# Optimization experiments

Hardware: AMD Instinct MI355X
Metric: run time of the kernel (lower is better)

## Reference

```python
import jax, jax.numpy as jnp
import numpy as np

N_NODES = 50000
N_PAIRS = 625000
F = 128

def setup_inputs() -> dict:
    key = jax.random.key(0)
    k1, k2, k3, k4, k5 = jax.random.split(key, 5)
    x = jax.random.normal(k1, (N_NODES, F), dtype=jnp.float32)
    alpha_ij = jax.random.normal(k2, (N_PAIRS,), dtype=jnp.float32)
    idx_i = jax.random.randint(k3, (N_PAIRS,), 0, N_NODES, dtype=jnp.int32)
    idx_j = jax.random.randint(k4, (N_PAIRS,), 0, N_NODES, dtype=jnp.int32)
    # Dense(F, use_bias=False) kernel, shape (F_in, F_out)
    W = jax.random.normal(k5, (F, F), dtype=jnp.float32) / np.sqrt(F)
    return {"x": x, "alpha_ij": alpha_ij, "idx_i": idx_i, "idx_j": idx_j, "W": W}

def reference(x, alpha_ij, idx_i, idx_j, W):
    # dense projection on nodes (n,F) @ (F,F) -> (n,F)
    v = jnp.matmul(x, W)
    # gather neighbor values, scale by attention coeff: (n_pairs, F)
    msg = alpha_ij[:, None] * v[idx_j]
    # scatter-sum back to center atoms
    return jax.ops.segment_sum(msg, segment_ids=idx_i, num_segments=x.shape[0])
```

## Files before the change

### kernel.cpp

```cpp
#include <hip/hip_runtime.h>
#include <stdint.h>

#define FDIM 128
#define BR 64
#define NB_C 782
#define QC 1152
#define PPB 2048

typedef short  s8v   __attribute__((ext_vector_type(8)));
typedef float  f4v   __attribute__((ext_vector_type(4)));
typedef unsigned short u8v __attribute__((ext_vector_type(8)));

__device__ __forceinline__ unsigned short f2bf(float f) {
    union { float f; uint32_t u; } c; c.f = f;
    uint32_t u = c.u;
    return (unsigned short)((u + 0x7fffu + ((u >> 16) & 1u)) >> 16);
}
__device__ __forceinline__ float bflo2f(uint32_t g) {
    union { uint32_t u; float f; } c; c.u = g << 16; return c.f;
}
__device__ __forceinline__ float bfhi2f(uint32_t g) {
    union { uint32_t u; float f; } c; c.u = g & 0xffff0000u; return c.f;
}

__global__ __launch_bounds__(256) void prep(const float* __restrict__ W,
                                            unsigned short* __restrict__ Wt,
                                            int* __restrict__ gcur) {
    int i = blockIdx.x * 256 + threadIdx.x;
    if (i < FDIM * FDIM) {
        int n = i & 127, k = i >> 7;
        Wt[n * FDIM + k] = f2bf(W[k * FDIM + n]);
    }
    if (i < NB_C) gcur[i] = 0;
}

__global__ __launch_bounds__(256) void fused_gemm_pass1(
        const float* __restrict__ x,
        const unsigned short* __restrict__ Wt,
        unsigned short* __restrict__ v,
        const int* __restrict__ idx_i,
        const int* __restrict__ idx_j,
        const float* __restrict__ alpha,
        int* __restrict__ gcur,
        unsigned long long* __restrict__ qrec,
        int n_rows, int n_pairs, int PB) {
    __shared__ unsigned short As[BR][FDIM + 8];

    if ((int)blockIdx.x < PB) {
        __shared__ int hist[NB_C];
        __shared__ int base_s[NB_C];
        const int t = threadIdx.x;
        const int start = blockIdx.x * PPB;

        for (int b = t; b < NB_C; b += 256) hist[b] = 0;
        __syncthreads();

        unsigned long long rec[8];
        int bkt[8];
#pragma unroll
        for (int i = 0; i < 8; ++i) {
            int p = start + t + i * 256;
            bkt[i] = -1;
            if (p < n_pairs) {
                int ii = idx_i[p];
                int b  = ii >> 6;
                bkt[i] = b;
                rec[i] = (unsigned long long)(uint32_t)(idx_j[p] | ((ii & 63) << 16))
                       | ((unsigned long long)(uint32_t)__float_as_int(alpha[p]) << 32);
                atomicAdd(&hist[b], 1);
            }
        }
        __syncthreads();
        for (int b = t; b < NB_C; b += 256) {
            int h = hist[b];
            base_s[b] = (h > 0) ? atomicAdd(&gcur[b], h) : 0;
            hist[b] = 0;
        }
        __syncthreads();
#pragma unroll
        for (int i = 0; i < 8; ++i) {
            int b = bkt[i];
            if (b >= 0) {
                int lp  = atomicAdd(&hist[b], 1);
                int pos = base_s[b] + lp;
                if (pos < QC)
                    qrec[(size_t)b * QC + pos] = rec[i];
            }
        }
        return;
    }

    const int t = threadIdx.x;
    const int row0 = (blockIdx.x - PB) * BR;
    {
        int r  = t >> 2;
        int c0 = (t & 3) * 32;
        int grow = row0 + r;
        const float* src = x + (size_t)grow * FDIM + c0;
#pragma unroll
        for (int it = 0; it < 4; ++it) {
            float4 xa = make_float4(0.f, 0.f, 0.f, 0.f);
            float4 xb = make_float4(0.f, 0.f, 0.f, 0.f);
            if (grow < n_rows) {
                xa = *(const float4*)(src + it * 8);
                xb = *(const float4*)(src + it * 8 + 4);
            }
            u8v pk;
            pk[0] = f2bf(xa.x); pk[1] = f2bf(xa.y); pk[2] = f2bf(xa.z); pk[3] = f2bf(xa.w);
            pk[4] = f2bf(xb.x); pk[5] = f2bf(xb.y); pk[6] = f2bf(xb.z); pk[7] = f2bf(xb.w);
            *(u8v*)(&As[r][c0 + it * 8]) = pk;
        }
    }
    __syncthreads();

    const int w    = t >> 6;
    const int lane = t & 63;
    const int rt   = (w & 1) * 32;
    const int ct   = (w >> 1) * 64;
    const int lrow = lane & 15;
    const int kq   = (lane >> 4) * 8;

    f4v acc[2][4];
#pragma unroll
    for (int i = 0; i < 2; ++i)
#pragma unroll
        for (int j = 0; j < 4; ++j)
            acc[i][j] = (f4v){0.f, 0.f, 0.f, 0.f};

#pragma unroll
    for (int ks = 0; ks < 4; ++ks) {
        const int k0 = ks * 32 + kq;
        const unsigned short* wb = Wt + (size_t)(ct + lrow) * FDIM + k0;
        s8v b0 = *(const s8v*)(wb);
        s8v b1 = *(const s8v*)(wb + 16 * FDIM);
        s8v b2 = *(const s8v*)(wb + 32 * FDIM);
        s8v b3 = *(const s8v*)(wb + 48 * FDIM);
        s8v a0 = *(const s8v*)(&As[rt + lrow][k0]);
        s8v a1 = *(const s8v*)(&As[rt + 16 + lrow][k0]);
        acc[0][0] = __builtin_amdgcn_mfma_f32_16x16x32_bf16(a0, b0, acc[0][0], 0, 0, 0);
        acc[0][1] = __builtin_amdgcn_mfma_f32_16x16x32_bf16(a0, b1, acc[0][1], 0, 0, 0);
        acc[0][2] = __builtin_amdgcn_mfma_f32_16x16x32_bf16(a0, b2, acc[0][2], 0, 0, 0);
        acc[0][3] = __builtin_amdgcn_mfma_f32_16x16x32_bf16(a0, b3, acc[0][3], 0, 0, 0);
        acc[1][0] = __builtin_amdgcn_mfma_f32_16x16x32_bf16(a1, b0, acc[1][0], 0, 0, 0);
        acc[1][1] = __builtin_amdgcn_mfma_f32_16x16x32_bf16(a1, b1, acc[1][1], 0, 0, 0);
        acc[1][2] = __builtin_amdgcn_mfma_f32_16x16x32_bf16(a1, b2, acc[1][2], 0, 0, 0);
        acc[1][3] = __builtin_amdgcn_mfma_f32_16x16x32_bf16(a1, b3, acc[1][3], 0, 0, 0);
    }

    const int quad = lane >> 4;
#pragma unroll
    for (int i = 0; i < 2; ++i) {
#pragma unroll
        for (int r = 0; r < 4; ++r) {
            int row = row0 + rt + i * 16 + quad * 4 + r;
            if (row < n_rows) {
#pragma unroll
                for (int j = 0; j < 4; ++j) {
                    int col = ct + j * 16 + lrow;
                    v[(size_t)row * FDIM + col] = f2bf(acc[i][j][r]);
                }
            }
        }
    }
}

__global__ __launch_bounds__(512) void bucket_agg(
        const unsigned short* __restrict__ v,
        const int* __restrict__ gcur,
        const unsigned long long* __restrict__ qrec,
        float* __restrict__ out,
        int n_nodes) {
    __shared__ unsigned long long sraw[QC];
    __shared__ unsigned long long ssort[QC];
    __shared__ int cnt64[64];
    __shared__ int start[65];
    const int t = threadIdx.x;
    const int c = blockIdx.x;

    int nrec = gcur[c];
    nrec = (nrec > QC) ? QC : nrec;
    const unsigned long long* q = qrec + (size_t)c * QC;

    if (t < 64) cnt64[t] = 0;
    __syncthreads();
    for (int k = t; k < nrec; k += 512) {
        unsigned long long r = q[k];
        sraw[k] = r;
        atomicAdd(&cnt64[(int)((r >> 16) & 63)], 1);
    }
    __syncthreads();

    if (t < 64) {
        int v0 = cnt64[t];
        int s  = v0;
#pragma unroll
        for (int d = 1; d < 64; d <<= 1) {
            int n = __shfl_up(s, d);
            if (t >= d) s += n;
        }
        start[t]  = s - v0;
        cnt64[t]  = s - v0;
        if (t == 63) start[64] = s;
    }
    __syncthreads();

    for (int k = t; k < nrec; k += 512) {
        unsigned long long r = sraw[k];
        int off = (int)((r >> 16) & 63);
        int pos = atomicAdd(&cnt64[off], 1);
        ssort[pos] = r;
    }
    __syncthreads();

    const int wv   = t >> 6;
    const int lane = t & 63;
#pragma unroll 1
    for (int i = 0; i < 8; ++i) {
        const int off  = wv * 8 + i;
        const int node = c * 64 + off;
        const int s0 = start[off];
        const int s1 = start[off + 1];

        float ax = 0.f, ay = 0.f;
        int k = s0;
        for (; k + 4 <= s1; k += 4) {
            unsigned long long r0 = ssort[k];
            unsigned long long r1 = ssort[k + 1];
            unsigned long long r2 = ssort[k + 2];
            unsigned long long r3 = ssort[k + 3];
            int j0 = (int)(r0 & 0xffff), j1 = (int)(r1 & 0xffff);
            int j2 = (int)(r2 & 0xffff), j3 = (int)(r3 & 0xffff);
            float a0 = __int_as_float((int)(r0 >> 32));
            float a1 = __int_as_float((int)(r1 >> 32));
            float a2 = __int_as_float((int)(r2 >> 32));
            float a3 = __int_as_float((int)(r3 >> 32));
            uint32_t g0 = *(const uint32_t*)(v + (size_t)j0 * FDIM + lane * 2);
            uint32_t g1 = *(const uint32_t*)(v + (size_t)j1 * FDIM + lane * 2);
            uint32_t g2 = *(const uint32_t*)(v + (size_t)j2 * FDIM + lane * 2);
            uint32_t g3 = *(const uint32_t*)(v + (size_t)j3 * FDIM + lane * 2);
            ax += a0 * bflo2f(g0) + a1 * bflo2f(g1);
            ay += a0 * bfhi2f(g0) + a1 * bfhi2f(g1);
            ax += a2 * bflo2f(g2) + a3 * bflo2f(g3);
            ay += a2 * bfhi2f(g2) + a3 * bfhi2f(g3);
        }
        if (k + 2 <= s1) {
            unsigned long long r0 = ssort[k];
            unsigned long long r1 = ssort[k + 1];
            int j0 = (int)(r0 & 0xffff), j1 = (int)(r1 & 0xffff);
            float a0 = __int_as_float((int)(r0 >> 32));
            float a1 = __int_as_float((int)(r1 >> 32));
            uint32_t g0 = *(const uint32_t*)(v + (size_t)j0 * FDIM + lane * 2);
            uint32_t g1 = *(const uint32_t*)(v + (size_t)j1 * FDIM + lane * 2);
            ax += a0 * bflo2f(g0) + a1 * bflo2f(g1);
            ay += a0 * bfhi2f(g0) + a1 * bfhi2f(g1);
            k += 2;
        }
        if (k < s1) {
            unsigned long long r0 = ssort[k];
            int j0 = (int)(r0 & 0xffff);
            float a0 = __int_as_float((int)(r0 >> 32));
            uint32_t g0 = *(const uint32_t*)(v + (size_t)j0 * FDIM + lane * 2);
            ax += a0 * bflo2f(g0);
            ay += a0 * bfhi2f(g0);
        }
        if (node < n_nodes) {
            float2 r;
            r.x = ax;
            r.y = ay;
            *(float2*)(out + (size_t)node * FDIM + lane * 2) = r;
        }
    }
}

extern "C" void kernel_launch(void* const* d_in, const int* in_sizes, int n_in,
                              void* d_out, int out_size, void* d_ws, size_t ws_size,
                              hipStream_t stream) {
    const float* x     = (const float*)d_in[0];
    const float* alpha = (const float*)d_in[1];
    const int*   idx_i = (const int*)d_in[2];
    const int*   idx_j = (const int*)d_in[3];
    const float* W     = (const float*)d_in[4];

    const int n_nodes = in_sizes[0] / FDIM;
    const int n_pairs = in_sizes[1];

    char* ws = (char*)d_ws;
    size_t off = 0;
    auto carve = [&](size_t bytes) {
        char* p = ws + off;
        off += (bytes + 255) & ~(size_t)255;
        return p;
    };
    unsigned short* v  = (unsigned short*)carve((size_t)n_nodes * FDIM * sizeof(unsigned short));
    unsigned short* Wt = (unsigned short*)carve((size_t)FDIM * FDIM * sizeof(unsigned short));
    int*  gcur = (int*)carve((size_t)NB_C * sizeof(int));
    unsigned long long* qrec =
        (unsigned long long*)carve((size_t)NB_C * QC * sizeof(unsigned long long));
    float* out = (float*)d_out;

    prep<<<(FDIM * FDIM + 255) / 256, 256, 0, stream>>>(W, Wt, gcur);

    int GB = (n_nodes + BR - 1) / BR;
    int PB = (n_pairs + PPB - 1) / PPB;
    fused_gemm_pass1<<<PB + GB, 256, 0, stream>>>(x, Wt, v, idx_i, idx_j, alpha,
                                                  gcur, qrec, n_nodes, n_pairs, PB);

    bucket_agg<<<NB_C, 512, 0, stream>>>(v, gcur, qrec, out, n_nodes);
}
```

Baseline: 132.0 us.

## Reorder to aggregate bf16 x first, then apply W GEMM per bucket

Measured after the change: 146.6 us. +11.1%, slower.

```diff
diff --git a/kernel.cpp b/kernel.cpp
--- a/kernel.cpp
+++ b/kernel.cpp
@@ -2,10 +2,10 @@
 #include <stdint.h>
 
 #define FDIM 128
-#define BR 64
 #define NB_C 782
 #define QC 1152
 #define PPB 2048
+#define CONVB 782
 
 typedef short  s8v   __attribute__((ext_vector_type(8)));
 typedef float  f4v   __attribute__((ext_vector_type(4)));
@@ -34,17 +34,15 @@
     if (i < NB_C) gcur[i] = 0;
 }
 
-__global__ __launch_bounds__(256) void fused_gemm_pass1(
+__global__ __launch_bounds__(256) void convert_pass1(
         const float* __restrict__ x,
-        const unsigned short* __restrict__ Wt,
-        unsigned short* __restrict__ v,
+        unsigned short* __restrict__ xb,
         const int* __restrict__ idx_i,
         const int* __restrict__ idx_j,
         const float* __restrict__ alpha,
         int* __restrict__ gcur,
         unsigned long long* __restrict__ qrec,
         int n_rows, int n_pairs, int PB) {
-    __shared__ unsigned short As[BR][FDIM + 8];
 
     if ((int)blockIdx.x < PB) {
         __shared__ int hist[NB_C];
@@ -90,82 +88,23 @@
         return;
     }
 
-    const int t = threadIdx.x;
-    const int row0 = (blockIdx.x - PB) * BR;
-    {
-        int r  = t >> 2;
-        int c0 = (t & 3) * 32;
-        int grow = row0 + r;
-        const float* src = x + (size_t)grow * FDIM + c0;
-#pragma unroll
-        for (int it = 0; it < 4; ++it) {
-            float4 xa = make_float4(0.f, 0.f, 0.f, 0.f);
-            float4 xb = make_float4(0.f, 0.f, 0.f, 0.f);
-            if (grow < n_rows) {
-                xa = *(const float4*)(src + it * 8);
-                xb = *(const float4*)(src + it * 8 + 4);
-            }
-            u8v pk;
-            pk[0] = f2bf(xa.x); pk[1] = f2bf(xa.y); pk[2] = f2bf(xa.z); pk[3] = f2bf(xa.w);
-            pk[4] = f2bf(xb.x); pk[5] = f2bf(xb.y); pk[6] = f2bf(xb.z); pk[7] = f2bf(xb.w);
-            *(u8v*)(&As[r][c0 + it * 8]) = pk;
-        }
-    }
-    __syncthreads();
-
-    const int w    = t >> 6;
-    const int lane = t & 63;
-    const int rt   = (w & 1) * 32;
-    const int ct   = (w >> 1) * 64;
-    const int lrow = lane & 15;
-    const int kq   = (lane >> 4) * 8;
-
-    f4v acc[2][4];
-#pragma unroll
-    for (int i = 0; i < 2; ++i)
-#pragma unroll
-        for (int j = 0; j < 4; ++j)
-            acc[i][j] = (f4v){0.f, 0.f, 0.f, 0.f};
-
-#pragma unroll
-    for (int ks = 0; ks < 4; ++ks) {
-        const int k0 = ks * 32 + kq;
-        const unsigned short* wb = Wt + (size_t)(ct + lrow) * FDIM + k0;
-        s8v b0 = *(const s8v*)(wb);
-        s8v b1 = *(const s8v*)(wb + 16 * FDIM);
-        s8v b2 = *(const s8v*)(wb + 32 * FDIM);
-        s8v b3 = *(const s8v*)(wb + 48 * FDIM);
-        s8v a0 = *(const s8v*)(&As[rt + lrow][k0]);
-        s8v a1 = *(const s8v*)(&As[rt + 16 + lrow][k0]);
-        acc[0][0] = __builtin_amdgcn_mfma_f32_16x16x32_bf16(a0, b0, acc[0][0], 0, 0, 0);
-        acc[0][1] = __builtin_amdgcn_mfma_f32_16x16x32_bf16(a0, b1, acc[0][1], 0, 0, 0);
-        acc[0][2] = __builtin_amdgcn_mfma_f32_16x16x32_bf16(a0, b2, acc[0][2], 0, 0, 0);
-        acc[0][3] = __builtin_amdgcn_mfma_f32_16x16x32_bf16(a0, b3, acc[0][3], 0, 0, 0);
-        acc[1][0] = __builtin_amdgcn_mfma_f32_16x16x32_bf16(a1, b0, acc[1][0], 0, 0, 0);
-        acc[1][1] = __builtin_amdgcn_mfma_f32_16x16x32_bf16(a1, b1, acc[1][1], 0, 0, 0);
-        acc[1][2] = __builtin_amdgcn_mfma_f32_16x16x32_bf16(a1, b2, acc[1][2], 0, 0, 0);
-        acc[1][3] = __builtin_amdgcn_mfma_f32_16x16x32_bf16(a1, b3, acc[1][3], 0, 0, 0);
-    }
-
-    const int quad = lane >> 4;
-#pragma unroll
-    for (int i = 0; i < 2; ++i) {
-#pragma unroll
-        for (int r = 0; r < 4; ++r) {
-            int row = row0 + rt + i * 16 + quad * 4 + r;
-            if (row < n_rows) {
-#pragma unroll
-                for (int j = 0; j < 4; ++j) {
-                    int col = ct + j * 16 + lrow;
-                    v[(size_t)row * FDIM + col] = f2bf(acc[i][j][r]);
-                }
-            }
-        }
-    }
-}
-
-__global__ __launch_bounds__(512) void bucket_agg(
-        const unsigned short* __restrict__ v,
+    const long long total8 = (long long)n_rows * FDIM / 8;
+    long long i8 = (long long)((int)blockIdx.x - PB) * 256 + threadIdx.x;
+    const long long stride = (long long)CONVB * 256;
+    for (; i8 < total8; i8 += stride) {
+        const float* src = x + i8 * 8;
+        float4 a = ((const float4*)src)[0];
+        float4 b = ((const float4*)src)[1];
+        u8v pk;
+        pk[0] = f2bf(a.x); pk[1] = f2bf(a.y); pk[2] = f2bf(a.z); pk[3] = f2bf(a.w);
+        pk[4] = f2bf(b.x); pk[5] = f2bf(b.y); pk[6] = f2bf(b.z); pk[7] = f2bf(b.w);
+        *(u8v*)(xb + i8 * 8) = pk;
+    }
+}
+
+__global__ __launch_bounds__(512) void agg_gemm(
+        const unsigned short* __restrict__ xb,
+        const unsigned short* __restrict__ Wt,
         const int* __restrict__ gcur,
         const unsigned long long* __restrict__ qrec,
         float* __restrict__ out,
@@ -174,8 +113,11 @@
     __shared__ unsigned long long ssort[QC];
     __shared__ int cnt64[64];
     __shared__ int start[65];
-    const int t = threadIdx.x;
-    const int c = blockIdx.x;
+    __shared__ float sacc[64][FDIM + 4];
+    const int t    = threadIdx.x;
+    const int c    = blockIdx.x;
+    const int wv   = t >> 6;
+    const int lane = t & 63;
 
     int nrec = gcur[c];
     nrec = (nrec > QC) ? QC : nrec;
@@ -212,12 +154,9 @@
     }
     __syncthreads();
 
-    const int wv   = t >> 6;
-    const int lane = t & 63;
 #pragma unroll 1
     for (int i = 0; i < 8; ++i) {
-        const int off  = wv * 8 + i;
-        const int node = c * 64 + off;
+        const int off = wv * 8 + i;
         const int s0 = start[off];
         const int s1 = start[off + 1];
 
@@ -234,10 +173,10 @@
             float a1 = __int_as_float((int)(r1 >> 32));
             float a2 = __int_as_float((int)(r2 >> 32));
             float a3 = __int_as_float((int)(r3 >> 32));
-            uint32_t g0 = *(const uint32_t*)(v + (size_t)j0 * FDIM + lane * 2);
-            uint32_t g1 = *(const uint32_t*)(v + (size_t)j1 * FDIM + lane * 2);
-            uint32_t g2 = *(const uint32_t*)(v + (size_t)j2 * FDIM + lane * 2);
-            uint32_t g3 = *(const uint32_t*)(v + (size_t)j3 * FDIM + lane * 2);
+            uint32_t g0 = *(const uint32_t*)(xb + (size_t)j0 * FDIM + lane * 2);
+            uint32_t g1 = *(const uint32_t*)(xb + (size_t)j1 * FDIM + lane * 2);
+            uint32_t g2 = *(const uint32_t*)(xb + (size_t)j2 * FDIM + lane * 2);
+            uint32_t g3 = *(const uint32_t*)(xb + (size_t)j3 * FDIM + lane * 2);
             ax += a0 * bflo2f(g0) + a1 * bflo2f(g1);
             ay += a0 * bfhi2f(g0) + a1 * bfhi2f(g1);
             ax += a2 * bflo2f(g2) + a3 * bflo2f(g3);
@@ -249,8 +188,8 @@
             int j0 = (int)(r0 & 0xffff), j1 = (int)(r1 & 0xffff);
             float a0 = __int_as_float((int)(r0 >> 32));
             float a1 = __int_as_float((int)(r1 >> 32));
-            uint32_t g0 = *(const uint32_t*)(v + (size_t)j0 * FDIM + lane * 2);
-            uint32_t g1 = *(const uint32_t*)(v + (size_t)j1 * FDIM + lane * 2);
+            uint32_t g0 = *(const uint32_t*)(xb + (size_t)j0 * FDIM + lane * 2);
+            uint32_t g1 = *(const uint32_t*)(xb + (size_t)j1 * FDIM + lane * 2);
             ax += a0 * bflo2f(g0) + a1 * bflo2f(g1);
             ay += a0 * bfhi2f(g0) + a1 * bfhi2f(g1);
             k += 2;
@@ -259,15 +198,65 @@
             unsigned long long r0 = ssort[k];
             int j0 = (int)(r0 & 0xffff);
             float a0 = __int_as_float((int)(r0 >> 32));
-            uint32_t g0 = *(const uint32_t*)(v + (size_t)j0 * FDIM + lane * 2);
+            uint32_t g0 = *(const uint32_t*)(xb + (size_t)j0 * FDIM + lane * 2);
             ax += a0 * bflo2f(g0);
             ay += a0 * bfhi2f(g0);
         }
-        if (node < n_nodes) {
-            float2 r;
-            r.x = ax;
-            r.y = ay;
-            *(float2*)(out + (size_t)node * FDIM + lane * 2) = r;
+        sacc[off][lane * 2]     = ax;
+        sacc[off][lane * 2 + 1] = ay;
+    }
+    __syncthreads();
+
+    const int w    = wv;
+    const int rt   = (w & 3) * 16;
+    const int ct   = (w >> 2) * 64;
+    const int lrow = lane & 15;
+    const int kq   = (lane >> 4) * 8;
+
+    f4v acc[4];
+#pragma unroll
+    for (int j = 0; j < 4; ++j) acc[j] = (f4v){0.f, 0.f, 0.f, 0.f};
+
+#pragma unroll
+    for (int ks = 0; ks < 4; ++ks) {
+        const int k0 = ks * 32 + kq;
+        const float* ap = &sacc[rt + lrow][k0];
+        f4v f0 = *(const f4v*)(ap);
+        f4v f1 = *(const f4v*)(ap + 4);
+        s8v ahi, alo;
+#pragma unroll
+        for (int e = 0; e < 4; ++e) {
+            unsigned short h0 = f2bf(f0[e]);
+            unsigned short h1 = f2bf(f1[e]);
+            ahi[e]     = (short)h0;
+            ahi[e + 4] = (short)h1;
+            alo[e]     = (short)f2bf(f0[e] - bflo2f(h0));
+            alo[e + 4] = (short)f2bf(f1[e] - bflo2f(h1));
+        }
+        const unsigned short* wb = Wt + (size_t)(ct + lrow) * FDIM + k0;
+        s8v b0 = *(const s8v*)(wb);
+        s8v b1 = *(const s8v*)(wb + 16 * FDIM);
+        s8v b2 = *(const s8v*)(wb + 32 * FDIM);
+        s8v b3 = *(const s8v*)(wb + 48 * FDIM);
+        acc[0] = __builtin_amdgcn_mfma_f32_16x16x32_bf16(ahi, b0, acc[0], 0, 0, 0);
+        acc[1] = __builtin_amdgcn_mfma_f32_16x16x32_bf16(ahi, b1, acc[1], 0, 0, 0);
+        acc[2] = __builtin_amdgcn_mfma_f32_16x16x32_bf16(ahi, b2, acc[2], 0, 0, 0);
+        acc[3] = __builtin_amdgcn_mfma_f32_16x16x32_bf16(ahi, b3, acc[3], 0, 0, 0);
+        acc[0] = __builtin_amdgcn_mfma_f32_16x16x32_bf16(alo, b0, acc[0], 0, 0, 0);
+        acc[1] = __builtin_amdgcn_mfma_f32_16x16x32_bf16(alo, b1, acc[1], 0, 0, 0);
+        acc[2] = __builtin_amdgcn_mfma_f32_16x16x32_bf16(alo, b2, acc[2], 0, 0, 0);
+        acc[3] = __builtin_amdgcn_mfma_f32_16x16x32_bf16(alo, b3, acc[3], 0, 0, 0);
+    }
+
+    const int quad = lane >> 4;
+#pragma unroll
+    for (int j = 0; j < 4; ++j) {
+#pragma unroll
+        for (int r = 0; r < 4; ++r) {
+            int row  = rt + quad * 4 + r;
+            int node = c * 64 + row;
+            if (node < n_nodes)
+                out[(size_t)node * FDIM + ct + j * 16 + lrow] = acc[j][r];
         }
     }
 }
@@ -291,7 +280,7 @@
         off += (bytes + 255) & ~(size_t)255;
         return p;
     };
-    unsigned short* v  = (unsigned short*)carve((size_t)n_nodes * FDIM * sizeof(unsigned short));
+    unsigned short* xb = (unsigned short*)carve((size_t)n_nodes * FDIM * sizeof(unsigned short));
     unsigned short* Wt = (unsigned short*)carve((size_t)FDIM * FDIM * sizeof(unsigned short));
     int*  gcur = (int*)carve((size_t)NB_C * sizeof(int));
     unsigned long long* qrec =
@@ -300,10 +289,9 @@
 
     prep<<<(FDIM * FDIM + 255) / 256, 256, 0, stream>>>(W, Wt, gcur);
 
-    int GB = (n_nodes + BR - 1) / BR;
     int PB = (n_pairs + PPB - 1) / PPB;
-    fused_gemm_pass1<<<PB + GB, 256, 0, stream>>>(x, Wt, v, idx_i, idx_j, alpha,
+    convert_pass1<<<PB + CONVB, 256, 0, stream>>>(x, xb, idx_i, idx_j, alpha,
                                                   gcur, qrec, n_nodes, n_pairs, PB);
 
-    bucket_agg<<<NB_C, 512, 0, stream>>>(v, gcur, qrec, out, n_nodes);
-}
+    agg_gemm<<<NB_C, 512, 0, stream>>>(xb, Wt, gcur, qrec, out, n_nodes);
+}
```
